# Kernel tuning notes

Hardware: AMD Instinct MI355X
Metric: run time of the kernel (lower is better)

## Reference

```python
import jax, jax.numpy as jnp
import numpy as np

E = 1024      # embbed_size
NH = 64       # num_hiddens (per-head dim)
H = 16        # num_heads (NH*H == E)
B = 8192
S = 2
EPS = 1e-5


def setup_inputs() -> dict:
    key = jax.random.key(0)
    ks = jax.random.split(key, 20)
    g = lambda i, shape, scale: (jax.random.normal(ks[i], shape, dtype=jnp.float32) * scale)
    d = {
        "input": g(0, (B, S, E), 1.0),
        # attention projections (bias=False), torch Linear weight layout (out, in)
        "Wq": g(1, (NH * H, E), E ** -0.5),
        "Wk": g(2, (NH * H, E), E ** -0.5),
        "Wv": g(3, (NH * H, E), E ** -0.5),
        "Wo": g(4, (E, NH * H), E ** -0.5),
        # layernorms over [2, E]
        "ln1_w": jnp.ones((S, E), jnp.float32),
        "ln1_b": jnp.zeros((S, E), jnp.float32),
        "ln2_w": jnp.ones((S, E), jnp.float32),
        "ln2_b": jnp.zeros((S, E), jnp.float32),
        # ffn1 / ffn2: Linear(E,2E)+Tanh+Linear(2E,E)+Tanh (bias=True default)
        "f1w1": g(5, (2 * E, E), E ** -0.5), "f1b1": jnp.zeros((2 * E,), jnp.float32),
        "f1w2": g(6, (E, 2 * E), (2 * E) ** -0.5), "f1b2": jnp.zeros((E,), jnp.float32),
        "f2w1": g(7, (2 * E, E), E ** -0.5), "f2b1": jnp.zeros((2 * E,), jnp.float32),
        "f2w2": g(8, (E, 2 * E), (2 * E) ** -0.5), "f2b2": jnp.zeros((E,), jnp.float32),
    }
    return d


def _layernorm2d(x, w, b):
    # torch LayerNorm([2, E]): normalize jointly over the last TWO dims
    m = jnp.mean(x, axis=(-2, -1), keepdims=True)
    v = jnp.mean(jnp.square(x - m), axis=(-2, -1), keepdims=True)
    return (x - m) * jax.lax.rsqrt(v + EPS) * w + b


def _split_heads(x):
    # faithful to transpose_qkv: reshape(B,S,NH,H) then permute(0,3,1,2) -> (B,H,S,NH)
    return x.reshape(B, S, NH, H).transpose(0, 3, 1, 2)


def reference(input, Wq, Wk, Wv, Wo, ln1_w, ln1_b, ln2_w, ln2_b,
              f1w1, f1b1, f1w2, f1b2, f2w1, f2b1, f2w2, f2b2):
    xs = _layernorm2d(input, ln1_w, ln1_b)                 # (B,S,E)
    q = _split_heads(xs @ Wq.T)                            # (B,H,S,NH)
    k = _split_heads(xs @ Wk.T)
    v = _split_heads(xs @ Wv.T)
    att = jnp.einsum("bhsd,bhtd->bhst", q, k) / np.sqrt(NH)
    out = jnp.einsum("bhst,bhtd->bhsd", jax.nn.softmax(att, axis=-1), v)  # (B,H,S,NH)
    # permute(0,2,3,1) -> (B,S,NH,H), reshape -> (B,S,NH*H)
    concat = out.transpose(0, 2, 3, 1).reshape(B, S, NH * H)
    res = concat @ Wo.T                                    # (B,S,E)
    out1 = input + res
    out_s = _layernorm2d(out1, ln2_w, ln2_b)
    s0 = jnp.tanh(jnp.tanh(out_s[:, 0, :] @ f1w1.T + f1b1) @ f1w2.T + f1b2)
    s1 = jnp.tanh(jnp.tanh(out_s[:, 1, :] @ f2w1.T + f2b1) @ f2w2.T + f2b2)
    return jnp.stack((s0, s1), axis=1) + out1
```

## Files before the change

### kernel.cpp

```cpp
#include <hip/hip_runtime.h>
#include <hip/hip_bf16.h>
#include <stdint.h>


typedef __attribute__((ext_vector_type(8))) short short8;
typedef __attribute__((ext_vector_type(4))) float floatx4;

__device__ __forceinline__ float b2f(short s) {
  union { unsigned u; float f; } v;
  v.u = ((unsigned)(unsigned short)s) << 16;
  return v.f;
}
__device__ __forceinline__ short f2b(float f) {
  union { float f; unsigned u; } v;
  v.f = f;
  unsigned r = v.u + 0x7FFFu + ((v.u >> 16) & 1u);
  return (short)(r >> 16);
}
__device__ __forceinline__ float fast_tanh(float x) {
  float e = __expf(2.f * x);
  return 1.f - 2.f / (e + 1.f);
}
__device__ __forceinline__ void load16_lds(const void* g, void* l) {
  __builtin_amdgcn_global_load_lds(
      (__attribute__((address_space(1))) void*)(void*)g,
      (__attribute__((address_space(3))) void*)l, 16, 0, 0);
}

struct Src4 { const float* p[4]; };

__global__ __launch_bounds__(256) void cvt4_kernel(Src4 s,
                                                   short* __restrict__ y,
                                                   int sh) {
  const int i = blockIdx.x * 256 + threadIdx.x;
  const int seg = i >> sh;
  const int off = i & ((1 << sh) - 1);
  const float* x = s.p[seg];
  const float4 a = ((const float4*)x)[(size_t)off * 2];
  const float4 b = ((const float4*)x)[(size_t)off * 2 + 1];
  short8 r;
  r[0] = f2b(a.x); r[1] = f2b(a.y); r[2] = f2b(a.z); r[3] = f2b(a.w);
  r[4] = f2b(b.x); r[5] = f2b(b.y); r[6] = f2b(b.z); r[7] = f2b(b.w);
  ((short8*)y)[i] = r;
}

template <int EPI, int ZSEL>
__global__ __launch_bounds__(256, 4) void gemm_bt(
    const short* A, int lda, const short* W, int K, void* Cout, int ldc,
    const float* aux, int ld_aux, const float* bias, const short* res, int ldr,
    const short* Wz, const float* biasz, int a_zoff, int c_zoff) {
  __shared__ short As[128 * 64];
  __shared__ short Bs[128 * 64];
  const int tid = threadIdx.x;
  const int lane = tid & 63;
  const int wid = tid >> 6;
  const int l15 = lane & 15;
  const int l4 = lane >> 4;
  const int wm = (wid >> 1) * 64;
  const int wn = (wid & 1) * 64;
  const int bn0 = blockIdx.x * 128;
  const int bm0 = blockIdx.y * 128;

  const short* Wp = W;
  const float* bp = bias;
  int coff = 0;
  if (ZSEL && blockIdx.z) {
    Wp = Wz;
    bp = biasz;
    A += a_zoff;
    coff = c_zoff;
  }

  floatx4 zero = {0.f, 0.f, 0.f, 0.f};
  floatx4 acc[4][4];
#pragma unroll
  for (int i = 0; i < 4; ++i)
#pragma unroll
    for (int j = 0; j < 4; ++j) acc[i][j] = zero;

  const int r8 = lane >> 3;
  const int gsw = (lane & 7) ^ r8;
  const int aoff = r8 * lda + gsw * 8;
  const int boff = r8 * K + gsw * 8;
  const short* Ab = A + (size_t)bm0 * lda;
  const short* Bb = Wp + (size_t)bn0 * K;
  const int e0 = __builtin_amdgcn_readfirstlane(wid * 4);
  const int swz = l15 & 7;

  for (int k0 = 0; k0 < K; k0 += 64) {
#pragma unroll
    for (int t = 0; t < 4; ++t) {
      const int e = e0 + t;
      load16_lds(Ab + (size_t)e * 8 * lda + k0 + aoff, &As[e * 512]);
      load16_lds(Bb + (size_t)e * 8 * K + k0 + boff, &Bs[e * 512]);
    }
    __syncthreads();
#pragma unroll
    for (int kk = 0; kk < 2; ++kk) {
      const int ko = ((kk * 4 + l4) ^ swz) * 8;
      short8 av[4], bv[4];
#pragma unroll
      for (int i = 0; i < 4; ++i) {
        av[i] = *(const short8*)&As[(wm + i * 16 + l15) * 64 + ko];
        bv[i] = *(const short8*)&Bs[(wn + i * 16 + l15) * 64 + ko];
      }
#pragma unroll
      for (int i = 0; i < 4; ++i)
#pragma unroll
        for (int j = 0; j < 4; ++j)
          acc[i][j] = __builtin_amdgcn_mfma_f32_16x16x32_bf16(av[i], bv[j],
                                                              acc[i][j], 0, 0, 0);
    }
    __syncthreads();
  }

  const int mb = bm0 + wm + l4 * 4;
  const int nb = bn0 + wn + l15;
#pragma unroll
  for (int i = 0; i < 4; ++i) {
#pragma unroll
    for (int p = 0; p < 4; ++p) {
      const int r = mb + i * 16 + p;
#pragma unroll
      for (int j = 0; j < 4; ++j) {
        const int n = nb + j * 16;
        float c = acc[i][j][p];
        if (EPI == 0) {
          ((short*)Cout)[(size_t)r * ldc + n + coff] = f2b(c);
        } else if (EPI == 1) {
          ((short*)Cout)[(size_t)r * ldc + n + coff] =
              f2b(c + aux[(size_t)r * ld_aux + n]);
        } else if (EPI == 2) {
          ((short*)Cout)[(size_t)r * ldc + n + coff] =
              f2b(fast_tanh(c + bp[n]));
        } else {
          const float rv = b2f(res[(size_t)r * ldr + n + coff]);
          ((float*)Cout)[(size_t)r * ldc + n + coff] =
              fast_tanh(c + bp[n]) + rv;
        }
      }
    }
  }
}

template <int INBF16>
__global__ __launch_bounds__(256) void ln_kernel(const void* __restrict__ xin,
                                                 const float* __restrict__ w,
                                                 const float* __restrict__ bb,
                                                 short* __restrict__ y) {
  const int b = blockIdx.x;
  const int tid = threadIdx.x;
  const size_t base = (size_t)b * 2048 + tid * 8;
  float xv[8];
  if (INBF16) {
    short8 s = *(const short8*)((const short*)xin + base);
#pragma unroll
    for (int j = 0; j < 8; ++j) xv[j] = b2f(s[j]);
  } else {
    const float4 a = *(const float4*)((const float*)xin + base);
    const float4 c = *(const float4*)((const float*)xin + base + 4);
    xv[0] = a.x; xv[1] = a.y; xv[2] = a.z; xv[3] = a.w;
    xv[4] = c.x; xv[5] = c.y; xv[6] = c.z; xv[7] = c.w;
  }
  float sum = 0.f, sq = 0.f;
#pragma unroll
  for (int j = 0; j < 8; ++j) {
    sum += xv[j];
    sq += xv[j] * xv[j];
  }
  __shared__ float rs[8];
  const int lane = tid & 63, wid = tid >> 6;
#pragma unroll
  for (int off = 32; off; off >>= 1) {
    sum += __shfl_down(sum, off);
    sq += __shfl_down(sq, off);
  }
  if (lane == 0) {
    rs[wid] = sum;
    rs[4 + wid] = sq;
  }
  __syncthreads();
  const float stot = rs[0] + rs[1] + rs[2] + rs[3];
  const float qtot = rs[4] + rs[5] + rs[6] + rs[7];
  const float mean = stot * (1.f / 2048.f);
  const float rstd = rsqrtf(qtot * (1.f / 2048.f) - mean * mean + 1e-5f);
  const int wi = tid * 8;
  short8 r;
#pragma unroll
  for (int j = 0; j < 8; ++j)
    r[j] = f2b((xv[j] - mean) * rstd * w[wi + j] + bb[wi + j]);
  *(short8*)(y + base) = r;
}

__global__ __launch_bounds__(256) void attn_kernel(short* qkv) {
  __shared__ short sm[2][6][1032];
  __shared__ float sps[2][2][2][16];
  __shared__ float spp[2][2][2][16];
  const int tid = threadIdx.x;
  const int half = tid >> 7;
  const int t = tid & 127;
  const int b = blockIdx.x * 2 + half;
  const short* row0 = qkv + ((size_t)b * 2 + 0) * 3072;
  const short* row1 = qkv + ((size_t)b * 2 + 1) * 3072;
  const short* srcs[6] = {row0,        row1,        row0 + 1024,
                          row1 + 1024, row0 + 2048, row1 + 2048};
#pragma unroll
  for (int rr = 0; rr < 6; ++rr)
    *(short8*)&sm[half][rr][t * 8] = *(const short8*)(srcs[rr] + t * 8);
  __syncthreads();
  if (t < 64) {
    const int h = t & 15, comb = t >> 4;
    const int si = comb >> 1, ti = comb & 1;
    const short* qr = sm[half][si];
    const short* kr = sm[half][2 + ti];
    float a = 0.f;
#pragma unroll
    for (int d = 0; d < 64; ++d) a += b2f(qr[d * 16 + h]) * b2f(kr[d * 16 + h]);
    sps[half][si][ti][h] = a * 0.125f;
  }
  __syncthreads();
  if (t < 32) {
    const int h = t & 15, si = t >> 4;
    const float s0 = sps[half][si][0][h], s1 = sps[half][si][1][h];
    const float m = fmaxf(s0, s1);
    const float e0 = __expf(s0 - m), e1 = __expf(s1 - m);
    const float inv = 1.f / (e0 + e1);
    spp[half][si][0][h] = e0 * inv;
    spp[half][si][1][h] = e1 * inv;
  }
  __syncthreads();
#pragma unroll
  for (int si = 0; si < 2; ++si) {
    short8 r;
#pragma unroll
    for (int j = 0; j < 8; ++j) {
      const int e = t * 8 + j;
      const int h = e & 15;
      const float c = spp[half][si][0][h] * b2f(sm[half][4][e]) +
                      spp[half][si][1][h] * b2f(sm[half][5][e]);
      r[j] = f2b(c);
    }
    *(short8*)(qkv + ((size_t)b * 2 + si) * 3072 + t * 8) = r;
  }
}

extern "C" void kernel_launch(void* const* d_in, const int* in_sizes, int n_in,
                              void* d_out, int out_size, void* d_ws,
                              size_t ws_size, hipStream_t stream) {
  (void)in_sizes; (void)n_in; (void)out_size; (void)ws_size;
  const float* input = (const float*)d_in[0];
  const float* Wq = (const float*)d_in[1];
  const float* Wk = (const float*)d_in[2];
  const float* Wv = (const float*)d_in[3];
  const float* Wo = (const float*)d_in[4];
  const float* ln1w = (const float*)d_in[5];
  const float* ln1b = (const float*)d_in[6];
  const float* ln2w = (const float*)d_in[7];
  const float* ln2b = (const float*)d_in[8];
  const float* f1w1 = (const float*)d_in[9];
  const float* f1b1 = (const float*)d_in[10];
  const float* f1w2 = (const float*)d_in[11];
  const float* f1b2 = (const float*)d_in[12];
  const float* f2w1 = (const float*)d_in[13];
  const float* f2b1 = (const float*)d_in[14];
  const float* f2w2 = (const float*)d_in[15];
  const float* f2b2 = (const float*)d_in[16];
  float* out = (float*)d_out;
  char* ws = (char*)d_ws;

  const size_t MB = 1024 * 1024;
  dim3 blk(256);

  short* wqkv = (short*)ws;
  short* wo = (short*)(ws + 6 * MB);
  short* xs = (short*)(ws + 8 * MB);
  short* out1 = xs;
  short* qkvb = (short*)(ws + 40 * MB);

  {
    Src4 s{{Wq, Wk, Wv, Wo}};
    cvt4_kernel<<<2048, blk, 0, stream>>>(s, wqkv, 17);
  }
  ln_kernel<0><<<8192, blk, 0, stream>>>(input, ln1w, ln1b, xs);
  {
    dim3 g(24, 128);
    gemm_bt<0, 0><<<g, blk, 0, stream>>>(xs, 1024, wqkv, 1024, qkvb, 3072,
                                         nullptr, 0, nullptr, nullptr, 0,
                                         nullptr, nullptr, 0, 0);
  }
  attn_kernel<<<4096, blk, 0, stream>>>(qkvb);
  {
    dim3 g(8, 128);
    gemm_bt<1, 0><<<g, blk, 0, stream>>>(qkvb, 3072, wo, 1024, out1, 1024,
                                         input, 1024, nullptr, nullptr, 0,
                                         nullptr, nullptr, 0, 0);
  }

  short* fw1s0 = (short*)(ws + 40 * MB);
  short* fw1s1 = (short*)(ws + 44 * MB);
  short* fw2s0 = (short*)(ws + 48 * MB);
  short* fw2s1 = (short*)(ws + 52 * MB);
  short* hb = (short*)(ws + 56 * MB);
  short* outs = (short*)out;
  {
    Src4 s{{f1w1, f2w1, f1w2, f2w2}};
    cvt4_kernel<<<4096, blk, 0, stream>>>(s, fw1s0, 18);
  }
  ln_kernel<1><<<8192, blk, 0, stream>>>(out1, ln2w, ln2b, outs);
  {
    dim3 g1(16, 64, 2);
    gemm_bt<2, 1><<<g1, blk, 0, stream>>>(
        outs, 2048, fw1s0, 1024, hb, 4096, nullptr, 0, f1b1, nullptr, 0,
        fw1s1, f2b1, 1024, 2048);
    dim3 g2(8, 64, 2);
    gemm_bt<3, 1><<<g2, blk, 0, stream>>>(
        hb, 4096, fw2s0, 2048, out, 2048, nullptr, 0, f1b2, out1, 2048,
        fw2s1, f2b2, 2048, 1024);
  }
}
```

Baseline: 547.5 us.

## Replace GEMM with 256x256-tile double-buffered 8-wave kernel and XCD-aware block remap

Rewrites the bf16 GEMM to use 256x256 output tiles with 8 waves, 128 KB of dynamic LDS for double-buffered A/B stages, and global-to-LDS loads for the next k-slice issued between MFMA phases. The phases are interleaved with barriers and raised wave priority so loads overlap compute. Block IDs are remapped across 8 groups for chiplet/L2 locality. The larger tiles cut global traffic per FLOP. In exchange, occupancy is lower, register pressure is higher, and there are fewer blocks, so wave quantization gets worse on the smaller GEMMs.

```diff
diff --git a/kernel.cpp b/kernel.cpp
--- a/kernel.cpp
+++ b/kernel.cpp
@@ -45,21 +45,25 @@
 }
 
 template <int EPI, int ZSEL>
-__global__ __launch_bounds__(256, 4) void gemm_bt(
+__global__ __launch_bounds__(512, 2) void gemm256(
     const short* A, int lda, const short* W, int K, void* Cout, int ldc,
     const float* aux, int ld_aux, const float* bias, const short* res, int ldr,
     const short* Wz, const float* biasz, int a_zoff, int c_zoff) {
-  __shared__ short As[128 * 64];
-  __shared__ short Bs[128 * 64];
+  extern __shared__ short lds[];
   const int tid = threadIdx.x;
   const int lane = tid & 63;
   const int wid = tid >> 6;
   const int l15 = lane & 15;
   const int l4 = lane >> 4;
-  const int wm = (wid >> 1) * 64;
-  const int wn = (wid & 1) * 64;
-  const int bn0 = blockIdx.x * 128;
-  const int bm0 = blockIdx.y * 128;
+  const int wm = (wid >> 2) * 128;
+  const int wn = (wid & 3) * 64;
+
+  const int gx = gridDim.x;
+  const int nwg = gx * gridDim.y;
+  const int bid0 = blockIdx.y * gx + blockIdx.x;
+  const int bid = (bid0 & 7) * (nwg >> 3) + (bid0 >> 3);
+  const int bn0 = (bid % gx) * 256;
+  const int bm0 = (bid / gx) * 256;
 
   const short* Wp = W;
   const float* bp = bias;
@@ -72,9 +76,9 @@
   }
 
   floatx4 zero = {0.f, 0.f, 0.f, 0.f};
-  floatx4 acc[4][4];
-#pragma unroll
-  for (int i = 0; i < 4; ++i)
+  floatx4 acc[8][4];
+#pragma unroll
+  for (int i = 0; i < 8; ++i)
 #pragma unroll
     for (int j = 0; j < 4; ++j) acc[i][j] = zero;
 
@@ -87,37 +91,78 @@
   const int e0 = __builtin_amdgcn_readfirstlane(wid * 4);
   const int swz = l15 & 7;
 
-  for (int k0 = 0; k0 < K; k0 += 64) {
-#pragma unroll
-    for (int t = 0; t < 4; ++t) {
-      const int e = e0 + t;
-      load16_lds(Ab + (size_t)e * 8 * lda + k0 + aoff, &As[e * 512]);
-      load16_lds(Bb + (size_t)e * 8 * K + k0 + boff, &Bs[e * 512]);
-    }
-    __syncthreads();
-#pragma unroll
-    for (int kk = 0; kk < 2; ++kk) {
-      const int ko = ((kk * 4 + l4) ^ swz) * 8;
-      short8 av[4], bv[4];
-#pragma unroll
-      for (int i = 0; i < 4; ++i) {
-        av[i] = *(const short8*)&As[(wm + i * 16 + l15) * 64 + ko];
-        bv[i] = *(const short8*)&Bs[(wn + i * 16 + l15) * 64 + ko];
-      }
-#pragma unroll
-      for (int i = 0; i < 4; ++i)
-#pragma unroll
-        for (int j = 0; j < 4; ++j)
-          acc[i][j] = __builtin_amdgcn_mfma_f32_16x16x32_bf16(av[i], bv[j],
-                                                              acc[i][j], 0, 0, 0);
-    }
-    __syncthreads();
-  }
+  short* As0 = lds;
+  short* As1 = lds + 16384;
+  short* Bs0 = lds + 32768;
+  short* Bs1 = lds + 49152;
+
+#define STAGE_A(slotptr, t, tk0) \
+  load16_lds(Ab + (size_t)(e0 + (t)) * 8 * lda + (tk0) + aoff, \
+             (slotptr) + (e0 + (t)) * 512)
+#define STAGE_B(slotptr, t, tk0) \
+  load16_lds(Bb + (size_t)(e0 + (t)) * 8 * K + (tk0) + boff, \
+             (slotptr) + (e0 + (t)) * 512)
+
+  short8 av[4], bv[4];
+
+#define PHASE(Asl, Bsl, kk, mh, STAGE_STMT, DOWAIT)                          \
+  {                                                                          \
+    const int ko = (((kk)*4 + l4) ^ swz) * 8;                                \
+    if ((mh) == 0) {                                                         \
+      _Pragma("unroll") for (int j = 0; j < 4; ++j)                          \
+          bv[j] = *(const short8*)&(Bsl)[(wn + j * 16 + l15) * 64 + ko];     \
+    }                                                                        \
+    _Pragma("unroll") for (int i = 0; i < 4; ++i)                            \
+        av[i] = *(const short8*)&(Asl)[(wm + (mh)*64 + i * 16 + l15) * 64 +  \
+                                       ko];                                  \
+    STAGE_STMT;                                                              \
+    asm volatile("" ::: "memory");                                           \
+    __builtin_amdgcn_s_barrier();                                            \
+    __builtin_amdgcn_s_setprio(1);                                           \
+    _Pragma("unroll") for (int i = 0; i < 4; ++i)                            \
+        _Pragma("unroll") for (int j = 0; j < 4; ++j)                        \
+            acc[(mh)*4 + i][j] = __builtin_amdgcn_mfma_f32_16x16x32_bf16(    \
+                av[i], bv[j], acc[(mh)*4 + i][j], 0, 0, 0);                  \
+    __builtin_amdgcn_s_setprio(0);                                           \
+    if (DOWAIT) asm volatile("s_waitcnt vmcnt(0)" ::: "memory");             \
+    asm volatile("" ::: "memory");                                           \
+    __builtin_amdgcn_s_barrier();                                            \
+  }
+
+#pragma unroll
+  for (int t = 0; t < 4; ++t) {
+    STAGE_A(As0, t, 0);
+    STAGE_B(Bs0, t, 0);
+  }
+  asm volatile("s_waitcnt vmcnt(0)" ::: "memory");
+  __builtin_amdgcn_s_barrier();
+
+  const int nit = K >> 7;
+  for (int it = 0; it < nit; ++it) {
+    const int kodd = it * 128 + 64;
+    const int knext = it * 128 + 128;
+    const bool more = (it + 1 < nit);
+    PHASE(As0, Bs0, 0, 0, { STAGE_A(As1, 0, kodd); STAGE_B(Bs1, 0, kodd); }, 0)
+    PHASE(As0, Bs0, 0, 1, { STAGE_A(As1, 1, kodd); STAGE_B(Bs1, 1, kodd); }, 0)
+    PHASE(As0, Bs0, 1, 0, { STAGE_A(As1, 2, kodd); STAGE_B(Bs1, 2, kodd); }, 0)
+    PHASE(As0, Bs0, 1, 1, { STAGE_A(As1, 3, kodd); STAGE_B(Bs1, 3, kodd); }, 1)
+    PHASE(As1, Bs1, 0, 0,
+          { if (more) { STAGE_A(As0, 0, knext); STAGE_B(Bs0, 0, knext); } }, 0)
+    PHASE(As1, Bs1, 0, 1,
+          { if (more) { STAGE_A(As0, 1, knext); STAGE_B(Bs0, 1, knext); } }, 0)
+    PHASE(As1, Bs1, 1, 0,
+          { if (more) { STAGE_A(As0, 2, knext); STAGE_B(Bs0, 2, knext); } }, 0)
+    PHASE(As1, Bs1, 1, 1,
+          { if (more) { STAGE_A(As0, 3, knext); STAGE_B(Bs0, 3, knext); } }, 1)
+  }
+#undef PHASE
+#undef STAGE_A
+#undef STAGE_B
 
   const int mb = bm0 + wm + l4 * 4;
   const int nb = bn0 + wn + l15;
 #pragma unroll
-  for (int i = 0; i < 4; ++i) {
+  for (int i = 0; i < 8; ++i) {
 #pragma unroll
     for (int p = 0; p < 4; ++p) {
       const int r = mb + i * 16 + p;
@@ -270,6 +315,19 @@
 
   const size_t MB = 1024 * 1024;
   dim3 blk(256);
+  dim3 gblk(512);
+  const int GLDS = 131072;
+
+  {
+    auto set = [](const void* f) {
+      (void)hipFuncSetAttribute(f, hipFuncAttributeMaxDynamicSharedMemorySize,
+                                131072);
+    };
+    set((const void*)gemm256<0, 0>);
+    set((const void*)gemm256<1, 0>);
+    set((const void*)gemm256<2, 1>);
+    set((const void*)gemm256<3, 1>);
+  }
 
   short* wqkv = (short*)ws;
   short* wo = (short*)(ws + 6 * MB);
@@ -283,17 +341,17 @@
   }
   ln_kernel<0><<<8192, blk, 0, stream>>>(input, ln1w, ln1b, xs);
   {
-    dim3 g(24, 128);
-    gemm_bt<0, 0><<<g, blk, 0, stream>>>(xs, 1024, wqkv, 1024, qkvb, 3072,
-                                         nullptr, 0, nullptr, nullptr, 0,
-                                         nullptr, nullptr, 0, 0);
+    dim3 g(12, 64);
+    gemm256<0, 0><<<g, gblk, GLDS, stream>>>(xs, 1024, wqkv, 1024, qkvb, 3072,
+                                             nullptr, 0, nullptr, nullptr, 0,
+                                             nullptr, nullptr, 0, 0);
   }
   attn_kernel<<<4096, blk, 0, stream>>>(qkvb);
   {
-    dim3 g(8, 128);
-    gemm_bt<1, 0><<<g, blk, 0, stream>>>(qkvb, 3072, wo, 1024, out1, 1024,
-                                         input, 1024, nullptr, nullptr, 0,
-                                         nullptr, nullptr, 0, 0);
+    dim3 g(4, 64);
+    gemm256<1, 0><<<g, gblk, GLDS, stream>>>(qkvb, 3072, wo, 1024, out1, 1024,
+                                             input, 1024, nullptr, nullptr, 0,
+                                             nullptr, nullptr, 0, 0);
   }
 
   short* fw1s0 = (short*)(ws + 40 * MB);
@@ -308,12 +366,12 @@
   }
   ln_kernel<1><<<8192, blk, 0, stream>>>(out1, ln2w, ln2b, outs);
   {
-    dim3 g1(16, 64, 2);
-    gemm_bt<2, 1><<<g1, blk, 0, stream>>>(
+    dim3 g1(8, 32, 2);
+    gemm256<2, 1><<<g1, gblk, GLDS, stream>>>(
         outs, 2048, fw1s0, 1024, hb, 4096, nullptr, 0, f1b1, nullptr, 0,
         fw1s1, f2b1, 1024, 2048);
-    dim3 g2(8, 64, 2);
-    gemm_bt<3, 1><<<g2, blk, 0, stream>>>(
+    dim3 g2(4, 32, 2);
+    gemm256<3, 1><<<g2, gblk, GLDS, stream>>>(
         hb, 4096, fw2s0, 2048, out, 2048, nullptr, 0, f1b2, out1, 2048,
         fw2s1, f2b2, 2048, 1024);
   }
```

After: 525.7 us. -4.0%, faster.
